# Kernel optimization log

Hardware: AMD Instinct MI355X
Metric: run time of the kernel (lower is better)

The kernel has to match this reference:

```python
import jax, jax.numpy as jnp
import numpy as np

B, N, D_IN = 128, 128, 1024
H1, D_OUT = 256, 32
K = 8  # num_clusters


def setup_inputs() -> dict:
    key = jax.random.key(0)
    ks = jax.random.split(key, 3)
    x = jax.random.normal(ks[0], (B, N, D_IN), dtype=jnp.float32)
    W1 = jax.random.normal(ks[1], (D_IN, H1), dtype=jnp.float32) * (1.0 / np.sqrt(D_IN))
    b1 = jnp.zeros((H1,), jnp.float32)
    W2 = jax.random.normal(ks[2], (H1, D_OUT), dtype=jnp.float32) * (1.0 / np.sqrt(H1))
    b2 = jnp.zeros((D_OUT,), jnp.float32)
    return {"x": x, "W1": W1, "b1": b1, "W2": W2, "b2": b2}


def _mlp(x, W1, b1, W2, b2):
    # nn.Sequential(GELU, Linear(1024,256), GELU, Linear(256,32)); torch GELU default = exact erf
    h = jax.nn.gelu(x, approximate=False)
    h = h @ W1 + b1
    h = jax.nn.gelu(h, approximate=False)
    return h @ W2 + b2  # [B, N, 32]


def _ward_labels(feats, k):
    """Greedy ward-linkage agglomerative clustering of feats [n, d] -> int labels [n].
    Ward merge cost d(A,B) = |A||B|/(|A|+|B|) * ||c_A - c_B||^2 (Lance-Williams equiv)."""
    n = feats.shape[0]
    eye = jnp.eye(n, dtype=bool)

    def body(t, state):
        cents, sizes, lab = state
        sq = jnp.sum(cents * cents, axis=-1)
        d2 = jnp.maximum(sq[:, None] + sq[None, :] - 2.0 * (cents @ cents.T), 0.0)
        w = (sizes[:, None] * sizes[None, :]) / (sizes[:, None] + sizes[None, :] + 1e-30)
        active = sizes > 0
        valid = (active[:, None] & active[None, :]) & (~eye)
        Dm = jnp.where(valid, w * d2, jnp.inf)
        idx = jnp.argmin(Dm)
        i, j = idx // n, idx % n
        i2 = jnp.minimum(i, j)
        j2 = jnp.maximum(i, j)
        si, sj = sizes[i2], sizes[j2]
        newc = (cents[i2] * si + cents[j2] * sj) / (si + sj)
        cents = cents.at[i2].set(newc)
        sizes = sizes.at[i2].set(si + sj).at[j2].set(0.0)
        lab = jnp.where(lab == j2, i2, lab)
        return cents, sizes, lab

    init = (feats, jnp.ones((n,), feats.dtype), jnp.arange(n))
    cents, sizes, lab = jax.lax.fori_loop(0, n - k, body, init)
    # relabel surviving representative indices to 0..k-1 (ordered by index)
    rank = jnp.cumsum((sizes > 0).astype(jnp.int32)) - 1
    return rank[lab]


def reference(x, W1, b1, W2, b2):
    feats = _mlp(x, W1, b1, W2, b2)          # [B, N, 32]
    labels = jax.vmap(lambda f: _ward_labels(f, K))(feats)  # [B, N] int32
    return labels
```

## Files before the change

kernel.cpp:

```cpp
#include <hip/hip_runtime.h>
#include <math.h>

#define BB 128
#define NN 128
#define DIN 1024
#define H1 256
#define DOUT 32
#define KCL 8
#define NPTS 128
#define MROWS (BB*NN)
#define CSTR 130
#define RSTR 132
#define DEADKEY 0xFFFFFFFF00000000ull

__device__ __forceinline__ float gelu_exact(float v) {
    return 0.5f * v * (1.0f + erff(v * 0.70710678118654752f));
}

__device__ __forceinline__ unsigned long long mkkey(float v, int r, int j) {
    return ((unsigned long long)__float_as_uint(v) << 32) | (unsigned)((r << 7) | j);
}

__device__ __forceinline__ float readlanef(float v, int lane) {
    return __int_as_float(__builtin_amdgcn_readlane(__float_as_int(v), lane));
}

template<int CTRL, int RMASK>
__device__ __forceinline__ unsigned dpp_umin_step(unsigned v) {
    unsigned t = (unsigned)__builtin_amdgcn_update_dpp((int)v, (int)v, CTRL, RMASK, 0xf, false);
    return t < v ? t : v;
}
__device__ __forceinline__ unsigned wave_umin_bcast(unsigned v) {
    v = dpp_umin_step<0x111, 0xf>(v);
    v = dpp_umin_step<0x112, 0xf>(v);
    v = dpp_umin_step<0x114, 0xf>(v);
    v = dpp_umin_step<0x118, 0xf>(v);
    v = dpp_umin_step<0x142, 0xa>(v);
    v = dpp_umin_step<0x143, 0xc>(v);
    return (unsigned)__builtin_amdgcn_readlane((int)v, 63);
}
__device__ __forceinline__ unsigned half_umin(unsigned v) {
    v = dpp_umin_step<0x111, 0xf>(v);
    v = dpp_umin_step<0x112, 0xf>(v);
    v = dpp_umin_step<0x114, 0xf>(v);
    v = dpp_umin_step<0x118, 0xf>(v);
    v = dpp_umin_step<0x142, 0xa>(v);
    return v;
}

__global__ __launch_bounds__(256) void mlp1_kernel(const float* __restrict__ x,
                                                   const float* __restrict__ W1,
                                                   const float* __restrict__ b1,
                                                   float* __restrict__ h) {
    __shared__ float As[2][32][68];
    __shared__ float Bs[2][32][132];
    const int bm = blockIdx.x;
    const int bn = blockIdx.y;
    const int tid = threadIdx.x;
    const int tx = tid & 15, ty = tid >> 4;

    float acc[4][8];
#pragma unroll
    for (int i = 0; i < 4; ++i)
#pragma unroll
        for (int j = 0; j < 8; ++j) acc[i][j] = 0.f;

    const int arow = tid >> 2;
    const int ak8 = (tid & 3) * 8;
    const int bk = tid >> 3;
    const int bc16 = (tid & 7) * 16;

    const float* xrow = x + (size_t)(bm * 64 + arow) * DIN;
    const float* wbase = W1 + bn * 128;

    float4 av0 = *(const float4*)(xrow + ak8);
    float4 av1 = *(const float4*)(xrow + ak8 + 4);
    float4 wv[4];
#pragma unroll
    for (int i = 0; i < 4; ++i)
        wv[i] = *(const float4*)(wbase + (size_t)bk * H1 + bc16 + 4 * i);

    for (int t = 0; t < 32; ++t) {
        const int p = t & 1;
        As[p][ak8 + 0][arow] = gelu_exact(av0.x);
        As[p][ak8 + 1][arow] = gelu_exact(av0.y);
        As[p][ak8 + 2][arow] = gelu_exact(av0.z);
        As[p][ak8 + 3][arow] = gelu_exact(av0.w);
        As[p][ak8 + 4][arow] = gelu_exact(av1.x);
        As[p][ak8 + 5][arow] = gelu_exact(av1.y);
        As[p][ak8 + 6][arow] = gelu_exact(av1.z);
        As[p][ak8 + 7][arow] = gelu_exact(av1.w);
#pragma unroll
        for (int i = 0; i < 4; ++i)
            *(float4*)&Bs[p][bk][bc16 + 4 * i] = wv[i];
        if (t + 1 < 32) {
            const int kt = (t + 1) * 32;
            av0 = *(const float4*)(xrow + kt + ak8);
            av1 = *(const float4*)(xrow + kt + ak8 + 4);
#pragma unroll
            for (int i = 0; i < 4; ++i)
                wv[i] = *(const float4*)(wbase + (size_t)(kt + bk) * H1 + bc16 + 4 * i);
        }
        __syncthreads();
#pragma unroll
        for (int kk = 0; kk < 32; ++kk) {
            float a[4], b[8];
            *(float4*)&a[0] = *(const float4*)&As[p][kk][ty * 4];
            *(float4*)&b[0] = *(const float4*)&Bs[p][kk][tx * 4];
            *(float4*)&b[4] = *(const float4*)&Bs[p][kk][64 + tx * 4];
#pragma unroll
            for (int i = 0; i < 4; ++i)
#pragma unroll
                for (int j = 0; j < 8; ++j)
                    acc[i][j] = fmaf(a[i], b[j], acc[i][j]);
        }
    }

    const int row = bm * 64 + ty * 4;
    const int col = bn * 128 + tx * 4;
    float4 bias0 = *(const float4*)(b1 + col);
    float4 bias1 = *(const float4*)(b1 + col + 64);
#pragma unroll
    for (int i = 0; i < 4; ++i) {
        float4 o0, o1;
        o0.x = acc[i][0] + bias0.x;
        o0.y = acc[i][1] + bias0.y;
        o0.z = acc[i][2] + bias0.z;
        o0.w = acc[i][3] + bias0.w;
        o1.x = acc[i][4] + bias1.x;
        o1.y = acc[i][5] + bias1.y;
        o1.z = acc[i][6] + bias1.z;
        o1.w = acc[i][7] + bias1.w;
        *(float4*)(h + (size_t)(row + i) * H1 + col) = o0;
        *(float4*)(h + (size_t)(row + i) * H1 + col + 64) = o1;
    }
}

__global__ __launch_bounds__(256) void mlp2_kernel(const float* __restrict__ h,
                                                   const float* __restrict__ W2,
                                                   const float* __restrict__ b2,
                                                   float* __restrict__ feats) {
    __shared__ float hs[16][257];
    __shared__ float w2s[H1 * DOUT];
    const int blk = blockIdx.x;
    const int tid = threadIdx.x;

    for (int i = tid; i < (H1 * DOUT) / 4; i += 256) {
        ((float4*)w2s)[i] = ((const float4*)W2)[i];
    }
    const float* hb = h + (size_t)blk * 16 * H1;
    for (int i = tid; i < (16 * H1) / 4; i += 256) {
        float4 v = ((const float4*)hb)[i];
        int r = i >> 6;
        int c = (i & 63) * 4;
        hs[r][c + 0] = gelu_exact(v.x);
        hs[r][c + 1] = gelu_exact(v.y);
        hs[r][c + 2] = gelu_exact(v.z);
        hs[r][c + 3] = gelu_exact(v.w);
    }
    __syncthreads();

    const int col = tid & 31;
    const int r0 = (tid >> 5) * 2;
    float acc0 = 0.f, acc1 = 0.f;
    for (int k = 0; k < H1; ++k) {
        float w = w2s[k * DOUT + col];
        acc0 = fmaf(hs[r0 + 0][k], w, acc0);
        acc1 = fmaf(hs[r0 + 1][k], w, acc1);
    }
    float bias = b2[col];
    const int rowg = blk * 16 + r0;
    feats[(size_t)(rowg + 0) * DOUT + col] = acc0 + bias;
    feats[(size_t)(rowg + 1) * DOUT + col] = acc1 + bias;
}

__global__ __launch_bounds__(256) void ward_kernel(const float* __restrict__ feats,
                                                   int* __restrict__ out) {
    __shared__ __align__(16) float cost[NPTS * RSTR];
    __shared__ __align__(16) float G[NPTS * RSTR];
    __shared__ float centsT[32 * CSTR];
    __shared__ unsigned long long rowkey[NPTS];
    __shared__ float sqArr[NPTS];
    __shared__ float szsE[NPTS];
    __shared__ int rnk[NPTS];

    const int b = blockIdx.x;
    const int tid = threadIdx.x;
    const float* f = feats + (size_t)b * NPTS * DOUT;
    const float INF = __builtin_inff();

    for (int i = tid; i < NPTS * DOUT; i += 256) {
        int r = i >> 5, d = i & 31;
        centsT[d * CSTR + r] = f[i];
    }
    __syncthreads();
    if (tid < NPTS) {
        float s = 0.f;
#pragma unroll
        for (int d = 0; d < 32; ++d) {
            float v = centsT[d * CSTR + tid];
            s = fmaf(v, v, s);
        }
        sqArr[tid] = s;
    }
    __syncthreads();
    {
        int ti = tid >> 4, tj = tid & 15;
        int I0 = ti * 8, J0 = tj * 8;
        float acc[8][8];
#pragma unroll
        for (int u = 0; u < 8; ++u)
#pragma unroll
            for (int v = 0; v < 8; ++v) acc[u][v] = 0.f;
        for (int d = 0; d < 32; ++d) {
            float a[8], bb[8];
#pragma unroll
            for (int u = 0; u < 8; ++u) a[u] = centsT[d * CSTR + I0 + u];
#pragma unroll
            for (int v = 0; v < 8; ++v) bb[v] = centsT[d * CSTR + J0 + v];
#pragma unroll
            for (int u = 0; u < 8; ++u)
#pragma unroll
                for (int v = 0; v < 8; ++v)
                    acc[u][v] = fmaf(a[u], bb[v], acc[u][v]);
        }
#pragma unroll
        for (int u = 0; u < 8; ++u) {
#pragma unroll
            for (int v = 0; v < 8; ++v) {
                int i = I0 + u, j = J0 + v;
                G[i * RSTR + j] = acc[u][v];
                float d2 = sqArr[i] + sqArr[j] - 2.0f * acc[u][v];
                if (d2 < 0.f) d2 = 0.f;
                float w = (1.0f * 1.0f) / (1.0f + 1.0f + 1e-30f);
                cost[i * RSTR + j] = (i == j) ? INF : w * d2;
            }
        }
    }
    __syncthreads();
    if (tid < NPTS) {
        unsigned long long best = DEADKEY;
        for (int j = 0; j < NPTS; ++j) {
            float v = cost[tid * RSTR + j];
            unsigned long long k = mkkey(v, tid, j);
            if (k < best) best = k;
        }
        rowkey[tid] = best;
    }
    __syncthreads();

    if (tid >= 64) return;
    const int lane = tid;
    const int hh = lane & 31;
    const int r0 = lane * 2, r1 = lane * 2 + 1;

    unsigned long long k0 = rowkey[r0], k1 = rowkey[r1];
    float q0 = sqArr[r0], q1 = sqArr[r1];
    float s0 = 1.0f, s1 = 1.0f;
    int lab0 = r0, lab1 = r1;
    unsigned long long alive0 = ~0ull, alive1 = ~0ull;

    for (int it = 0; it < NPTS - KCL; ++it) {
        unsigned bv0 = (unsigned)(k0 >> 32), bv1 = (unsigned)(k1 >> 32);
        unsigned lmin = bv0 < bv1 ? bv0 : bv1;
        unsigned lflat = (bv0 <= bv1) ? (unsigned)(k0 & 0x3FFFu) : (unsigned)(k1 & 0x3FFFu);
        unsigned gmin = wave_umin_bcast(lmin);
        unsigned long long bmask = __ballot(lmin == gmin);
        int lsel = __ffsll(bmask) - 1;
        unsigned flat = (unsigned)__builtin_amdgcn_readlane((int)lflat, lsel);
        int ra = (int)(flat >> 7), ca = (int)(flat & 127u);
        const int i2 = ra < ca ? ra : ca;
        const int j2 = ra < ca ? ca : ra;

        float2 gi = *(const float2*)&G[i2 * RSTR + r0];
        float2 gj = *(const float2*)&G[j2 * RSTR + r0];

        float si = readlanef((i2 & 1) ? s1 : s0, i2 >> 1);
        float sj = readlanef((j2 & 1) ? s1 : s0, j2 >> 1);
        const float snew = si + sj;
        const float invs = 1.0f / snew;
        const float wa = si * invs, wb = sj * invs;

        int arg0 = (int)(k0 & 127u), arg1 = (int)(k1 & 127u);
        bool d0 = (s0 > 0.f) && r0 != i2 && r0 != j2 && (arg0 == i2 || arg0 == j2);
        bool d1 = (s1 > 0.f) && r1 != i2 && r1 != j2 && (arg1 == i2 || arg1 == j2);
        unsigned long long m0 = __ballot(d0), m1 = __ballot(d1);

        float Gii = readlanef((i2 & 1) ? gi.y : gi.x, i2 >> 1);
        float Gij = readlanef((i2 & 1) ? gj.y : gj.x, i2 >> 1);
        float Gjj = readlanef((j2 & 1) ? gj.y : gj.x, j2 >> 1);
        float dotA = wa * Gii + wb * Gij;
        float dotB = wa * Gij + wb * Gjj;
        float qn = wa * dotA + wb * dotB;

        float dot0 = wa * gi.x + wb * gj.x;
        float dot1 = wa * gi.y + wb * gj.y;

        if (lab0 == j2) lab0 = i2;
        if (lab1 == j2) lab1 = i2;
        if (r0 == i2) s0 = snew; else if (r0 == j2) { s0 = 0.f; k0 = DEADKEY; }
        if (r1 == i2) s1 = snew; else if (r1 == j2) { s1 = 0.f; k1 = DEADKEY; }
        if (j2 < 64) alive0 &= ~(1ull << j2); else alive1 &= ~(1ull << (j2 - 64));
        if (r0 == i2) { dot0 = qn; q0 = qn; }
        if (r1 == i2) { dot1 = qn; q1 = qn; }

        *(float2*)&G[i2 * RSTR + r0] = make_float2(dot0, dot1);
        G[r0 * RSTR + i2] = dot0;
        G[r1 * RSTR + i2] = dot1;

        bool w0 = (s0 > 0.f) && r0 != i2 && r0 != j2;
        bool w1 = (s1 > 0.f) && r1 != i2 && r1 != j2;
        unsigned cb0 = 0xFFFFFFFFu, cb1 = 0xFFFFFFFFu;
        if (w0) {
            float d2 = q0 + qn - 2.0f * dot0;
            if (d2 < 0.f) d2 = 0.f;
            float w = (s0 * snew) / (s0 + snew + 1e-30f);
            float v0 = w * d2;
            cost[r0 * RSTR + i2] = v0;
            cost[i2 * RSTR + r0] = v0;
            cb0 = __float_as_uint(v0);
            if (!d0) {
                unsigned long long nk = mkkey(v0, r0, i2);
                if (nk < k0) k0 = nk;
            }
        }
        if (w1) {
            float d2 = q1 + qn - 2.0f * dot1;
            if (d2 < 0.f) d2 = 0.f;
            float w = (s1 * snew) / (s1 + snew + 1e-30f);
            float v1 = w * d2;
            cost[r1 * RSTR + i2] = v1;
            cost[i2 * RSTR + r1] = v1;
            cb1 = __float_as_uint(v1);
            if (!d1) {
                unsigned long long nk = mkkey(v1, r1, i2);
                if (nk < k1) k1 = nk;
            }
        }
        {
            unsigned lm = cb0 < cb1 ? cb0 : cb1;
            int lcol = (cb0 <= cb1) ? r0 : r1;
            unsigned gm = wave_umin_bcast(lm);
            unsigned long long mk2 = __ballot(lm == gm);
            int ls = __ffsll(mk2) - 1;
            int col = __builtin_amdgcn_readlane(lcol, ls);
            unsigned long long ki2 = ((unsigned long long)gm << 32) | (unsigned)((i2 << 7) | col);
            if (r0 == i2) k0 = ki2;
            if (r1 == i2) k1 = ki2;
        }

        unsigned long long mm0 = m0, mm1 = m1;
        while (mm0 | mm1) {
            int rA, rB;
            bool hasB = false;
            if (mm0) { int t = __ffsll(mm0) - 1; rA = 2 * t; mm0 &= mm0 - 1; }
            else     { int t = __ffsll(mm1) - 1; rA = 2 * t + 1; mm1 &= mm1 - 1; }
            if (mm0) { int t = __ffsll(mm0) - 1; rB = 2 * t; mm0 &= mm0 - 1; hasB = true; }
            else if (mm1) { int t = __ffsll(mm1) - 1; rB = 2 * t + 1; mm1 &= mm1 - 1; hasB = true; }
            else rB = rA;

            int r = (lane < 32) ? rA : rB;
            float4 cv = *(const float4*)&cost[r * RSTR + 4 * hh];
            unsigned long long word = (hh < 16) ? alive0 : alive1;
            unsigned nib = (unsigned)(word >> ((4 * hh) & 63)) & 0xFu;
            unsigned e0 = (nib & 1u) ? __float_as_uint(cv.x) : 0xFFFFFFFFu;
            unsigned e1 = (nib & 2u) ? __float_as_uint(cv.y) : 0xFFFFFFFFu;
            unsigned e2 = (nib & 4u) ? __float_as_uint(cv.z) : 0xFFFFFFFFu;
            unsigned e3 = (nib & 8u) ? __float_as_uint(cv.w) : 0xFFFFFFFFu;
            unsigned m = e0; int c = 0;
            if (e1 < m) { m = e1; c = 1; }
            if (e2 < m) { m = e2; c = 2; }
            if (e3 < m) { m = e3; c = 3; }
            int lcol = 4 * hh + c;
            unsigned hm = half_umin(m);
            unsigned vA = (unsigned)__builtin_amdgcn_readlane((int)hm, 31);
            unsigned vB = (unsigned)__builtin_amdgcn_readlane((int)hm, 63);
            unsigned vref = (lane < 32) ? vA : vB;
            unsigned long long msk = __ballot(m == vref);
            int laneA = __ffsll(msk & 0xFFFFFFFFull) - 1;
            int laneB = 32 + __ffsll(msk >> 32) - 1;
            int colA = __builtin_amdgcn_readlane(lcol, laneA);
            int colB = __builtin_amdgcn_readlane(lcol, laneB);
            unsigned long long keyA = ((unsigned long long)vA << 32) | (unsigned)((rA << 7) | colA);
            unsigned long long keyB = ((unsigned long long)vB << 32) | (unsigned)((rB << 7) | colB);
            if (lane == (rA >> 1)) { if (rA & 1) k1 = keyA; else k0 = keyA; }
            if (hasB && lane == (rB >> 1)) { if (rB & 1) k1 = keyB; else k0 = keyB; }
        }
    }

    szsE[r0] = s0;
    szsE[r1] = s1;
    __asm__ volatile("s_waitcnt lgkmcnt(0)" ::: "memory");
    if (lane == 0) {
        int c = 0;
        for (int i = 0; i < NPTS; ++i) rnk[i] = (szsE[i] > 0.f) ? c++ : -1;
    }
    __asm__ volatile("s_waitcnt lgkmcnt(0)" ::: "memory");
    out[b * NPTS + r0] = rnk[lab0];
    out[b * NPTS + r1] = rnk[lab1];
}

extern "C" void kernel_launch(void* const* d_in, const int* in_sizes, int n_in,
                              void* d_out, int out_size, void* d_ws, size_t ws_size,
                              hipStream_t stream) {
    const float* x  = (const float*)d_in[0];
    const float* W1 = (const float*)d_in[1];
    const float* b1 = (const float*)d_in[2];
    const float* W2 = (const float*)d_in[3];
    const float* b2 = (const float*)d_in[4];

    float* h = (float*)d_ws;
    float* feats = h + (size_t)MROWS * H1;
    int* out = (int*)d_out;

    mlp1_kernel<<<dim3(MROWS / 64, H1 / 128), 256, 0, stream>>>(x, W1, b1, h);
    mlp2_kernel<<<MROWS / 16, 256, 0, stream>>>(h, W2, b2, feats);
    ward_kernel<<<BB, 256, 0, stream>>>(feats, out);
}
```

Baseline: 451.7 us.

## Split GELU into separate pass, shrink GEMM tiles, and restructure ward row-min update

Adds a standalone elementwise GELU kernel writing a pre-activated copy of x to workspace when it has room; the first GEMM then reads that copy instead of applying erf-based GELU inside its tile loop. The GEMM also drops from 64x128 double-buffered tiles to 64x64 single-buffered tiles with a 4x4 micro-tile, doubling the grid. In the ward loop, the wave-wide reduction that rebuilt the merged row's key is removed and that row is instead pushed through the existing row-rescan loop. The trade is an extra 64 MB write and read for the GELU copy plus less register reuse per FMA, in exchange for fewer redundant erf evaluations and more blocks.

```diff
diff --git a/kernel.cpp b/kernel.cpp
--- a/kernel.cpp
+++ b/kernel.cpp
@@ -48,91 +48,95 @@
     return v;
 }
 
-__global__ __launch_bounds__(256) void mlp1_kernel(const float* __restrict__ x,
+__global__ __launch_bounds__(256) void gelu_kernel(const float* __restrict__ x,
+                                                   float* __restrict__ gx, int n4) {
+    int i = blockIdx.x * 256 + threadIdx.x;
+    const int stride = gridDim.x * 256;
+    for (; i < n4; i += stride) {
+        float4 v = ((const float4*)x)[i];
+        v.x = gelu_exact(v.x);
+        v.y = gelu_exact(v.y);
+        v.z = gelu_exact(v.z);
+        v.w = gelu_exact(v.w);
+        ((float4*)gx)[i] = v;
+    }
+}
+
+template<bool FUSE>
+__global__ __launch_bounds__(256) void mlp1_kernel(const float* __restrict__ xin,
                                                    const float* __restrict__ W1,
                                                    const float* __restrict__ b1,
                                                    float* __restrict__ h) {
-    __shared__ float As[2][32][68];
-    __shared__ float Bs[2][32][132];
+    __shared__ float As[32][68];
+    __shared__ float Bs[32][68];
     const int bm = blockIdx.x;
     const int bn = blockIdx.y;
     const int tid = threadIdx.x;
     const int tx = tid & 15, ty = tid >> 4;
 
-    float acc[4][8];
-#pragma unroll
-    for (int i = 0; i < 4; ++i)
-#pragma unroll
-        for (int j = 0; j < 8; ++j) acc[i][j] = 0.f;
+    float acc[4][4] = {{0.f}};
 
     const int arow = tid >> 2;
-    const int ak8 = (tid & 3) * 8;
-    const int bk = tid >> 3;
-    const int bc16 = (tid & 7) * 16;
-
-    const float* xrow = x + (size_t)(bm * 64 + arow) * DIN;
-    const float* wbase = W1 + bn * 128;
-
-    float4 av0 = *(const float4*)(xrow + ak8);
-    float4 av1 = *(const float4*)(xrow + ak8 + 4);
-    float4 wv[4];
-#pragma unroll
-    for (int i = 0; i < 4; ++i)
-        wv[i] = *(const float4*)(wbase + (size_t)bk * H1 + bc16 + 4 * i);
-
-    for (int t = 0; t < 32; ++t) {
-        const int p = t & 1;
-        As[p][ak8 + 0][arow] = gelu_exact(av0.x);
-        As[p][ak8 + 1][arow] = gelu_exact(av0.y);
-        As[p][ak8 + 2][arow] = gelu_exact(av0.z);
-        As[p][ak8 + 3][arow] = gelu_exact(av0.w);
-        As[p][ak8 + 4][arow] = gelu_exact(av1.x);
-        As[p][ak8 + 5][arow] = gelu_exact(av1.y);
-        As[p][ak8 + 6][arow] = gelu_exact(av1.z);
-        As[p][ak8 + 7][arow] = gelu_exact(av1.w);
-#pragma unroll
-        for (int i = 0; i < 4; ++i)
-            *(float4*)&Bs[p][bk][bc16 + 4 * i] = wv[i];
-        if (t + 1 < 32) {
-            const int kt = (t + 1) * 32;
-            av0 = *(const float4*)(xrow + kt + ak8);
-            av1 = *(const float4*)(xrow + kt + ak8 + 4);
+    const int acol4 = (tid & 3) * 4;
+    const int brow = tid >> 4;
+    const int bcol4 = (tid & 15) * 4;
+
+    const float* xrow = xin + (size_t)(bm * 64 + arow) * DIN;
+    const float* wbase = W1 + bn * 64;
+
+    for (int kt = 0; kt < DIN; kt += 32) {
+        float4 a0 = *(const float4*)(xrow + kt + acol4);
+        float4 a1 = *(const float4*)(xrow + kt + 16 + acol4);
+        float4 w0 = *(const float4*)(wbase + (size_t)(kt + brow) * H1 + bcol4);
+        float4 w1 = *(const float4*)(wbase + (size_t)(kt + 16 + brow) * H1 + bcol4);
+        __syncthreads();
+        if (FUSE) {
+            As[acol4 + 0][arow] = gelu_exact(a0.x);
+            As[acol4 + 1][arow] = gelu_exact(a0.y);
+            As[acol4 + 2][arow] = gelu_exact(a0.z);
+            As[acol4 + 3][arow] = gelu_exact(a0.w);
+            As[16 + acol4 + 0][arow] = gelu_exact(a1.x);
+            As[16 + acol4 + 1][arow] = gelu_exact(a1.y);
+            As[16 + acol4 + 2][arow] = gelu_exact(a1.z);
+            As[16 + acol4 + 3][arow] = gelu_exact(a1.w);
+        } else {
+            As[acol4 + 0][arow] = a0.x;
+            As[acol4 + 1][arow] = a0.y;
+            As[acol4 + 2][arow] = a0.z;
+            As[acol4 + 3][arow] = a0.w;
+            As[16 + acol4 + 0][arow] = a1.x;
+            As[16 + acol4 + 1][arow] = a1.y;
+            As[16 + acol4 + 2][arow] = a1.z;
+            As[16 + acol4 + 3][arow] = a1.w;
+        }
+        *(float4*)&Bs[brow][bcol4] = w0;
+        *(float4*)&Bs[16 + brow][bcol4] = w1;
+        __syncthreads();
+#pragma unroll
+        for (int kk = 0; kk < 32; ++kk) {
+            float4 a = *(const float4*)&As[kk][ty * 4];
+            float4 b = *(const float4*)&Bs[kk][tx * 4];
+            float ar[4] = {a.x, a.y, a.z, a.w};
+            float br[4] = {b.x, b.y, b.z, b.w};
 #pragma unroll
             for (int i = 0; i < 4; ++i)
-                wv[i] = *(const float4*)(wbase + (size_t)(kt + bk) * H1 + bc16 + 4 * i);
-        }
-        __syncthreads();
-#pragma unroll
-        for (int kk = 0; kk < 32; ++kk) {
-            float a[4], b[8];
-            *(float4*)&a[0] = *(const float4*)&As[p][kk][ty * 4];
-            *(float4*)&b[0] = *(const float4*)&Bs[p][kk][tx * 4];
-            *(float4*)&b[4] = *(const float4*)&Bs[p][kk][64 + tx * 4];
-#pragma unroll
-            for (int i = 0; i < 4; ++i)
-#pragma unroll
-                for (int j = 0; j < 8; ++j)
-                    acc[i][j] = fmaf(a[i], b[j], acc[i][j]);
+#pragma unroll
+                for (int j = 0; j < 4; ++j)
+                    acc[i][j] = fmaf(ar[i], br[j], acc[i][j]);
         }
     }
 
     const int row = bm * 64 + ty * 4;
-    const int col = bn * 128 + tx * 4;
-    float4 bias0 = *(const float4*)(b1 + col);
-    float4 bias1 = *(const float4*)(b1 + col + 64);
+    const int col = bn * 64 + tx * 4;
+    float4 bias = *(const float4*)(b1 + col);
 #pragma unroll
     for (int i = 0; i < 4; ++i) {
-        float4 o0, o1;
-        o0.x = acc[i][0] + bias0.x;
-        o0.y = acc[i][1] + bias0.y;
-        o0.z = acc[i][2] + bias0.z;
-        o0.w = acc[i][3] + bias0.w;
-        o1.x = acc[i][4] + bias1.x;
-        o1.y = acc[i][5] + bias1.y;
-        o1.z = acc[i][6] + bias1.z;
-        o1.w = acc[i][7] + bias1.w;
-        *(float4*)(h + (size_t)(row + i) * H1 + col) = o0;
-        *(float4*)(h + (size_t)(row + i) * H1 + col + 64) = o1;
+        float4 o;
+        o.x = acc[i][0] + bias.x;
+        o.y = acc[i][1] + bias.y;
+        o.z = acc[i][2] + bias.z;
+        o.w = acc[i][3] + bias.w;
+        *(float4*)(h + (size_t)(row + i) * H1 + col) = o;
     }
 }
 
@@ -310,7 +314,6 @@
 
         bool w0 = (s0 > 0.f) && r0 != i2 && r0 != j2;
         bool w1 = (s1 > 0.f) && r1 != i2 && r1 != j2;
-        unsigned cb0 = 0xFFFFFFFFu, cb1 = 0xFFFFFFFFu;
         if (w0) {
             float d2 = q0 + qn - 2.0f * dot0;
             if (d2 < 0.f) d2 = 0.f;
@@ -318,7 +321,6 @@
             float v0 = w * d2;
             cost[r0 * RSTR + i2] = v0;
             cost[i2 * RSTR + r0] = v0;
-            cb0 = __float_as_uint(v0);
             if (!d0) {
                 unsigned long long nk = mkkey(v0, r0, i2);
                 if (nk < k0) k0 = nk;
@@ -331,30 +333,20 @@
             float v1 = w * d2;
             cost[r1 * RSTR + i2] = v1;
             cost[i2 * RSTR + r1] = v1;
-            cb1 = __float_as_uint(v1);
             if (!d1) {
                 unsigned long long nk = mkkey(v1, r1, i2);
                 if (nk < k1) k1 = nk;
             }
         }
-        {
-            unsigned lm = cb0 < cb1 ? cb0 : cb1;
-            int lcol = (cb0 <= cb1) ? r0 : r1;
-            unsigned gm = wave_umin_bcast(lm);
-            unsigned long long mk2 = __ballot(lm == gm);
-            int ls = __ffsll(mk2) - 1;
-            int col = __builtin_amdgcn_readlane(lcol, ls);
-            unsigned long long ki2 = ((unsigned long long)gm << 32) | (unsigned)((i2 << 7) | col);
-            if (r0 == i2) k0 = ki2;
-            if (r1 == i2) k1 = ki2;
-        }
-
+
+        bool pi = true;
         unsigned long long mm0 = m0, mm1 = m1;
-        while (mm0 | mm1) {
+        while (pi | (mm0 != 0ull) | (mm1 != 0ull)) {
             int rA, rB;
             bool hasB = false;
-            if (mm0) { int t = __ffsll(mm0) - 1; rA = 2 * t; mm0 &= mm0 - 1; }
-            else     { int t = __ffsll(mm1) - 1; rA = 2 * t + 1; mm1 &= mm1 - 1; }
+            if (pi) { rA = i2; pi = false; }
+            else if (mm0) { int t = __ffsll(mm0) - 1; rA = 2 * t; mm0 &= mm0 - 1; }
+            else { int t = __ffsll(mm1) - 1; rA = 2 * t + 1; mm1 &= mm1 - 1; }
             if (mm0) { int t = __ffsll(mm0) - 1; rB = 2 * t; mm0 &= mm0 - 1; hasB = true; }
             else if (mm1) { int t = __ffsll(mm1) - 1; rB = 2 * t + 1; mm1 &= mm1 - 1; hasB = true; }
             else rB = rA;
@@ -411,9 +403,18 @@
 
     float* h = (float*)d_ws;
     float* feats = h + (size_t)MROWS * H1;
+    float* gx = feats + (size_t)MROWS * DOUT;
     int* out = (int*)d_out;
 
-    mlp1_kernel<<<dim3(MROWS / 64, H1 / 128), 256, 0, stream>>>(x, W1, b1, h);
+    const size_t need = ((size_t)MROWS * H1 + (size_t)MROWS * DOUT + (size_t)MROWS * DIN) * 4;
+    const bool use_gx = ws_size >= need;
+
+    if (use_gx) {
+        gelu_kernel<<<2048, 256, 0, stream>>>(x, gx, MROWS * DIN / 4);
+        mlp1_kernel<false><<<dim3(MROWS / 64, H1 / 64), 256, 0, stream>>>(gx, W1, b1, h);
+    } else {
+        mlp1_kernel<true><<<dim3(MROWS / 64, H1 / 64), 256, 0, stream>>>(x, W1, b1, h);
+    }
     mlp2_kernel<<<MROWS / 16, 256, 0, stream>>>(h, W2, b2, feats);
     ward_kernel<<<BB, 256, 0, stream>>>(feats, out);
 }
```

After: 431.0 us. -4.6%, faster.
